# Optimization experiments

Measured on AMD Instinct MI355X. Metric: run time of the kernel, lower is better.

## Reference

```python
import jax, jax.numpy as jnp
import numpy as np

B, S_T, P, D = 2, 8, 1369, 1024
S_STUDENT = 4
R = 128    # num_ref_samples
NS = 128   # num_shared_samples
K = 4      # topk
STUDENT_FRAMES = (0, 2, 4, 6)
EXTRA_FRAMES = (1, 3, 5, 7)   # teacher-only frames
HUBER_DELTA = 1.0
W1 = W2 = W3 = 1.0


def setup_inputs() -> dict:
    key = jax.random.key(0)
    k1, k2, k3, k4 = jax.random.split(key, 4)
    teacher_feats = jax.random.normal(k1, (B, S_T, P, D), dtype=jnp.float32)
    student_feats = jax.random.normal(k2, (B, S_STUDENT, P, D), dtype=jnp.float32)
    ref_perm = jax.random.permutation(k3, P)[:R].astype(jnp.int32)
    shared_perm = jax.random.permutation(k4, P)[:NS].astype(jnp.int32)
    return {"teacher_feats": teacher_feats, "student_feats": student_feats,
            "ref_perm": ref_perm, "shared_perm": shared_perm}


def _unit(x, eps):
    # F.normalize(x, dim=-1, eps=eps)
    n = jnp.linalg.norm(x, axis=-1, keepdims=True)
    return x / jnp.maximum(n, eps)


def _huber(pred, target):
    d = pred - target
    ad = jnp.abs(d)
    return jnp.where(ad < HUBER_DELTA, 0.5 * d * d, HUBER_DELTA * (ad - 0.5 * HUBER_DELTA))


def reference(teacher_feats, student_feats, ref_perm, shared_perm):
    t = jax.lax.stop_gradient(teacher_feats)  # teacher is always detached
    eps = 1e-8

    ref_t = t[:, STUDENT_FRAMES[0], ref_perm, :]        # [B,R,D]
    ref_s = student_feats[:, 0, ref_perm, :]            # [B,R,D]

    # top-K most similar teacher patches across extra frames
    extra_t = t[:, jnp.array(EXTRA_FRAMES)].reshape(B, len(EXTRA_FRAMES) * P, D)  # [B,M,D]
    sim = jnp.einsum('brd,bmd->brm', _unit(ref_t, 1e-12), _unit(extra_t, 1e-12))
    _, idx = jax.lax.top_k(sim, K)                      # [B,R,K]
    sim_high = jnp.take_along_axis(
        extra_t, idx.reshape(B, R * K)[:, :, None], axis=1).reshape(B, R, K, D)

    # vertex-ref / vertex-simhigh legs that don't depend on the shared frame
    b1_t = _unit(sim_high - ref_t[:, :, None, :], eps)  # [B,R,K,D]
    b1_s = _unit(sim_high - ref_s[:, :, None, :], eps)
    u2_t = _unit(ref_t[:, :, None, :] - sim_high, eps)  # [B,R,K,D]
    u2_s = _unit(ref_s[:, :, None, :] - sim_high, eps)

    s1 = jnp.float32(0.0)
    s2 = jnp.float32(0.0)
    s3 = jnp.float32(0.0)
    for f, t_idx in enumerate(STUDENT_FRAMES[1:]):
        sh_t = t[:, t_idx, shared_perm, :]              # [B,S,D]
        sh_s = student_feats[:, f + 1, shared_perm, :]  # [B,S,D]

        # angle1: vertex = ref; cos(shared-ref, simhigh-ref)
        a1_t = jnp.einsum('brsd,brkd->brsk', _unit(sh_t[:, None] - ref_t[:, :, None], eps), b1_t)
        a1_s = jnp.einsum('brsd,brkd->brsk', _unit(sh_s[:, None] - ref_s[:, :, None], eps), b1_s)
        s1 = s1 + _huber(a1_s, jax.lax.stop_gradient(a1_t)).sum()

        # angle2: vertex = sim_high; cos(ref-simhigh, shared-simhigh)
        v2_t = _unit(sh_t[:, None, :, None, :] - sim_high[:, :, None], eps)  # [B,R,S,K,D]
        v2_s = _unit(sh_s[:, None, :, None, :] - sim_high[:, :, None], eps)
        a2_t = jnp.einsum('brkd,brskd->brsk', u2_t, v2_t)
        a2_s = jnp.einsum('brkd,brskd->brsk', u2_s, v2_s)
        s2 = s2 + _huber(a2_s, jax.lax.stop_gradient(a2_t)).sum()

        # angle3: vertex = shared; cos(ref-shared, simhigh-shared)
        u3_t = _unit(ref_t[:, :, None] - sh_t[:, None], eps)                 # [B,R,S,D]
        u3_s = _unit(ref_s[:, :, None] - sh_s[:, None], eps)
        v3_t = _unit(sim_high[:, :, None] - sh_t[:, None, :, None, :], eps)  # [B,R,S,K,D]
        v3_s = _unit(sim_high[:, :, None] - sh_s[:, None, :, None, :], eps)
        a3_t = jnp.einsum('brsd,brskd->brsk', u3_t, v3_t)
        a3_s = jnp.einsum('brsd,brskd->brsk', u3_s, v3_s)
        s3 = s3 + _huber(a3_s, jax.lax.stop_gradient(a3_t)).sum()

    total = B * R * NS * K * len(STUDENT_FRAMES[1:])
    return W1 * s1 / total + W2 * s2 / total + W3 * s3 / total
```

## Files before the change

### kernel.cpp

```cpp
#include <hip/hip_runtime.h>
#include <float.h>

#define B_  2
#define ST_ 8
#define SS_ 4
#define P_  1369
#define D_  1024
#define R_  128
#define NS_ 128
#define K_  4
#define M_  5476

#define OFF_INVN  0u
#define OFF_REFT  11008u
#define OFF_REFS  (OFF_REFT + 262144u)
#define OFF_PRRT  (OFF_REFS + 262144u)
#define OFF_PRRS  (OFF_PRRT + 256u)
#define OFF_IDX   (OFF_PRRS + 256u)
#define OFF_PRST  (OFF_IDX + 1024u)
#define OFF_PRSS  (OFF_PRST + 1024u)
#define OFF_PSS   (OFF_PRSS + 1024u)
#define OFF_IB1T  (OFF_PSS + 1024u)
#define OFF_IB1S  (OFF_IB1T + 1024u)
#define OFF_NSH   (OFF_IB1S + 1024u)
#define OFF_CANDV (OFF_NSH + 1536u)
#define OFF_CANDI (OFF_CANDV + 4096u)
#define OFF_C     (OFF_CANDI + 4096u)
#define CP_       1401856u

#define NA_BLOCKS 2738
#define NB_BLOCKS 384
#define NC_BLOCKS 256

__device__ __forceinline__ float dot4(const float4 a, const float4 b) {
  return a.x*b.x + a.y*b.y + a.z*b.z + a.w*b.w;
}

__global__ __launch_bounds__(256) void k_prep0(const float* __restrict__ teacher,
                                               const float* __restrict__ student,
                                               const int* __restrict__ ref_perm,
                                               const int* __restrict__ shared_perm,
                                               float* __restrict__ invn,
                                               float* __restrict__ nsh,
                                               float* __restrict__ reft,
                                               float* __restrict__ refs,
                                               float* __restrict__ prrt,
                                               float* __restrict__ prrs) {
  const int bid = blockIdx.x;
  const int t = threadIdx.x;
  if (bid < NA_BLOCKS) {
    int row = bid * 4 + (t >> 6);
    int lane = t & 63;
    if (row >= B_ * M_) return;
    int b = row / M_, m = row % M_;
    int j = m / P_, p = m % P_;
    const float* src = teacher + (((size_t)b * ST_ + 1 + 2 * j) * P_ + p) * D_;
    float s = 0.f;
    #pragma unroll
    for (int it = 0; it < 4; ++it) {
      float4 v = *(const float4*)(src + (it * 64 + lane) * 4);
      s += dot4(v, v);
    }
    for (int o = 32; o; o >>= 1) s += __shfl_down(s, o);
    if (lane == 0) invn[row] = 1.f / fmaxf(sqrtf(s), 1e-12f);
  } else if (bid < NA_BLOCKS + NB_BLOCKS) {
    int row = (bid - NA_BLOCKS) * 4 + (t >> 6);
    int lane = t & 63;
    if (row >= 2 * B_ * 3 * NS_) return;
    int rid = row % (B_ * 3 * NS_);
    int is_stu = row / (B_ * 3 * NS_);
    int b = rid / (3 * NS_);
    int rem = rid % (3 * NS_);
    int f = rem / NS_, s = rem % NS_;
    int p = shared_perm[s];
    const float* src = is_stu
        ? student + (((size_t)b * SS_ + 1 + f) * P_ + p) * D_
        : teacher + (((size_t)b * ST_ + 2 + 2 * f) * P_ + p) * D_;
    float acc = 0.f;
    #pragma unroll
    for (int it = 0; it < 4; ++it) {
      float4 v = *(const float4*)(src + (it * 64 + lane) * 4);
      acc += dot4(v, v);
    }
    for (int o = 32; o; o >>= 1) acc += __shfl_down(acc, o);
    if (lane == 0) nsh[row] = acc;
  } else {
    int br = bid - (NA_BLOCKS + NB_BLOCKS);
    int b = br / R_, r = br % R_;
    int p = ref_perm[r];
    const float* st = teacher + (((size_t)b * ST_ + 0) * P_ + p) * D_;
    const float* ss = student + (((size_t)b * SS_ + 0) * P_ + p) * D_;
    float* dt = reft + (size_t)br * D_;
    float* dsp = refs + (size_t)br * D_;
    float4 vt = *(const float4*)(st + t * 4);
    float4 vs = *(const float4*)(ss + t * 4);
    *(float4*)(dt + t * 4) = vt;
    *(float4*)(dsp + t * 4) = vs;
    float at = dot4(vt, vt);
    float as = dot4(vs, vs);
    for (int o = 32; o; o >>= 1) { at += __shfl_down(at, o); as += __shfl_down(as, o); }
    __shared__ float red[16];
    int w = t >> 6, lane = t & 63;
    if (lane == 0) { red[w] = at; red[8 + w] = as; }
    __syncthreads();
    if (t == 0) {
      prrt[br] = red[0] + red[1] + red[2] + red[3];
      prrs[br] = red[8] + red[9] + red[10] + red[11];
    }
  }
}

__global__ __launch_bounds__(256) void k_sim_gemm(const float* __restrict__ teacher,
                                                  const float* __restrict__ reft,
                                                  float* __restrict__ Cp) {
  const int bid = blockIdx.x;
  const int kq  = bid & 3;
  const int rest = bid >> 2;
  const int b   = rest / 172;
  const int rem = rest % 172;
  const int rt  = rem / 86;
  const int mt  = rem % 86;
  const int r0 = rt * 64, m0 = mt * 64;
  __shared__ __align__(16) float Al[32 * 68];
  __shared__ __align__(16) float El[32 * 68];
  const int t = threadIdx.x;
  const int tx = t & 15, ty = t >> 4;
  const int lr = t >> 3;
  const int lk = (t & 7) * 4;
  const float* arow0 = reft + (size_t)(b * R_ + r0 + lr) * D_;
  const float* arow1 = reft + (size_t)(b * R_ + r0 + 32 + lr) * D_;
  const float* erow0; const float* erow1; bool ev0, ev1;
  {
    int m = m0 + lr; ev0 = m < M_;
    int mm = ev0 ? m : 0; int j = mm / P_, p = mm % P_;
    erow0 = teacher + (((size_t)b * ST_ + 1 + 2 * j) * P_ + p) * D_;
    m = m0 + 32 + lr; ev1 = m < M_;
    mm = ev1 ? m : 0; j = mm / P_; p = mm % P_;
    erow1 = teacher + (((size_t)b * ST_ + 1 + 2 * j) * P_ + p) * D_;
  }
  float acc[4][4];
  #pragma unroll
  for (int i = 0; i < 4; ++i)
    #pragma unroll
    for (int j = 0; j < 4; ++j) acc[i][j] = 0.f;

  const int kbeg = kq * 256, kend = kbeg + 256;
  for (int kc = kbeg; kc < kend; kc += 32) {
    __syncthreads();
    float4 a0 = *(const float4*)(arow0 + kc + lk);
    float4 a1 = *(const float4*)(arow1 + kc + lk);
    float4 e0 = ev0 ? *(const float4*)(erow0 + kc + lk) : make_float4(0, 0, 0, 0);
    float4 e1 = ev1 ? *(const float4*)(erow1 + kc + lk) : make_float4(0, 0, 0, 0);
    Al[(lk + 0) * 68 + lr] = a0.x; Al[(lk + 1) * 68 + lr] = a0.y;
    Al[(lk + 2) * 68 + lr] = a0.z; Al[(lk + 3) * 68 + lr] = a0.w;
    Al[(lk + 0) * 68 + 32 + lr] = a1.x; Al[(lk + 1) * 68 + 32 + lr] = a1.y;
    Al[(lk + 2) * 68 + 32 + lr] = a1.z; Al[(lk + 3) * 68 + 32 + lr] = a1.w;
    El[(lk + 0) * 68 + lr] = e0.x; El[(lk + 1) * 68 + lr] = e0.y;
    El[(lk + 2) * 68 + lr] = e0.z; El[(lk + 3) * 68 + lr] = e0.w;
    El[(lk + 0) * 68 + 32 + lr] = e1.x; El[(lk + 1) * 68 + 32 + lr] = e1.y;
    El[(lk + 2) * 68 + 32 + lr] = e1.z; El[(lk + 3) * 68 + 32 + lr] = e1.w;
    __syncthreads();
    #pragma unroll
    for (int kk = 0; kk < 32; ++kk) {
      float4 av = *(const float4*)&Al[kk * 68 + ty * 4];
      float4 ev = *(const float4*)&El[kk * 68 + tx * 4];
      acc[0][0] += av.x * ev.x; acc[0][1] += av.x * ev.y; acc[0][2] += av.x * ev.z; acc[0][3] += av.x * ev.w;
      acc[1][0] += av.y * ev.x; acc[1][1] += av.y * ev.y; acc[1][2] += av.y * ev.z; acc[1][3] += av.y * ev.w;
      acc[2][0] += av.z * ev.x; acc[2][1] += av.z * ev.y; acc[2][2] += av.z * ev.z; acc[2][3] += av.z * ev.w;
      acc[3][0] += av.w * ev.x; acc[3][1] += av.w * ev.y; acc[3][2] += av.w * ev.z; acc[3][3] += av.w * ev.w;
    }
  }
  const int mbase = m0 + tx * 4;
  float* cbase = Cp + (size_t)kq * CP_;
  #pragma unroll
  for (int i = 0; i < 4; ++i) {
    int r = r0 + ty * 4 + i;
    float* crow = cbase + (size_t)(b * R_ + r) * M_;
    if (mbase + 3 < M_) {
      *(float4*)(crow + mbase) = make_float4(acc[i][0], acc[i][1], acc[i][2], acc[i][3]);
    } else {
      if (mbase + 0 < M_) crow[mbase + 0] = acc[i][0];
      if (mbase + 1 < M_) crow[mbase + 1] = acc[i][1];
      if (mbase + 2 < M_) crow[mbase + 2] = acc[i][2];
      if (mbase + 3 < M_) crow[mbase + 3] = acc[i][3];
    }
  }
}

__device__ __forceinline__ void topk_insert(float v, int m, float bv[4], int bi[4]) {
  bool better3 = (v > bv[3]) || (v == bv[3] && m < bi[3]);
  if (!better3) return;
  int pos = 3;
  while (pos > 0) {
    bool better = (v > bv[pos - 1]) || (v == bv[pos - 1] && m < bi[pos - 1]);
    if (better) { bv[pos] = bv[pos - 1]; bi[pos] = bi[pos - 1]; --pos; }
    else break;
  }
  bv[pos] = v; bi[pos] = m;
}

__global__ __launch_bounds__(256) void k_topk1(const float* __restrict__ Cp,
                                               const float* __restrict__ invn,
                                               float* __restrict__ candv,
                                               int* __restrict__ candi) {
  int bid = blockIdx.x;
  int br = bid >> 2, q = bid & 3;
  int b = br / R_;
  const float* r0 = Cp + 0 * (size_t)CP_ + (size_t)br * M_;
  const float* r1 = Cp + 1 * (size_t)CP_ + (size_t)br * M_;
  const float* r2 = Cp + 2 * (size_t)CP_ + (size_t)br * M_;
  const float* r3 = Cp + 3 * (size_t)CP_ + (size_t)br * M_;
  const float* w = invn + (size_t)b * M_;
  const int mbeg = q * 1369, mend = mbeg + 1369;
  int t = threadIdx.x;
  float bv[4] = {-FLT_MAX, -FLT_MAX, -FLT_MAX, -FLT_MAX};
  int   bi[4] = {0x7fffffff, 0x7fffffff, 0x7fffffff, 0x7fffffff};
  for (int m = mbeg + t; m < mend; m += 256) {
    float v = ((r0[m] + r1[m]) + (r2[m] + r3[m])) * w[m];
    topk_insert(v, m, bv, bi);
  }
  #pragma unroll
  for (int o = 1; o < 64; o <<= 1) {
    float ov[4]; int oi[4];
    #pragma unroll
    for (int qq = 0; qq < 4; ++qq) {
      ov[qq] = __shfl_xor(bv[qq], o);
      oi[qq] = __shfl_xor(bi[qq], o);
    }
    #pragma unroll
    for (int qq = 0; qq < 4; ++qq) topk_insert(ov[qq], oi[qq], bv, bi);
  }
  __shared__ float sv[16];
  __shared__ int   si[16];
  int wv = t >> 6, lane = t & 63;
  if (lane == 0) {
    #pragma unroll
    for (int qq = 0; qq < 4; ++qq) { sv[wv * 4 + qq] = bv[qq]; si[wv * 4 + qq] = bi[qq]; }
  }
  __syncthreads();
  if (t == 0) {
    float tv[4] = {-FLT_MAX, -FLT_MAX, -FLT_MAX, -FLT_MAX};
    int   ti[4] = {0x7fffffff, 0x7fffffff, 0x7fffffff, 0x7fffffff};
    #pragma unroll
    for (int e = 0; e < 16; ++e) topk_insert(sv[e], si[e], tv, ti);
    #pragma unroll
    for (int qq = 0; qq < 4; ++qq) { candv[bid * 4 + qq] = tv[qq]; candi[bid * 4 + qq] = ti[qq]; }
  }
}

__global__ __launch_bounds__(256) void k_prep(const float* __restrict__ teacher,
                                              const float* __restrict__ reft,
                                              const float* __restrict__ refs,
                                              const float* __restrict__ candv,
                                              const int* __restrict__ candi,
                                              int* __restrict__ idxout,
                                              float* __restrict__ prst,
                                              float* __restrict__ prss,
                                              float* __restrict__ pss,
                                              float* __restrict__ ib1t,
                                              float* __restrict__ ib1s) {
  int br = blockIdx.x;
  int b = br / R_;
  int t = threadIdx.x;
  __shared__ int sidx[4];
  if (t < 64) {
    float v = -FLT_MAX; int ix = 0x7fffffff;
    if (t < 16) { v = candv[br * 16 + t]; ix = candi[br * 16 + t]; }
    float bv[4] = {v, -FLT_MAX, -FLT_MAX, -FLT_MAX};
    int   bi[4] = {ix, 0x7fffffff, 0x7fffffff, 0x7fffffff};
    #pragma unroll
    for (int o = 1; o <= 8; o <<= 1) {
      float ov[4]; int oi[4];
      #pragma unroll
      for (int q = 0; q < 4; ++q) {
        ov[q] = __shfl_xor(bv[q], o);
        oi[q] = __shfl_xor(bi[q], o);
      }
      #pragma unroll
      for (int q = 0; q < 4; ++q) topk_insert(ov[q], oi[q], bv, bi);
    }
    if (t == 0) {
      #pragma unroll
      for (int q = 0; q < 4; ++q) { sidx[q] = bi[q]; idxout[br * 4 + q] = bi[q]; }
    }
  }
  __syncthreads();
  int w = t >> 6, lane = t & 63;
  int m = sidx[w];
  int j = m / P_, p = m % P_;
  const float* sim = teacher + (((size_t)b * ST_ + 1 + 2 * j) * P_ + p) * D_;
  const float* rt = reft + (size_t)br * D_;
  const float* rs = refs + (size_t)br * D_;
  float s_ss = 0, s_rt = 0, s_rs = 0, s_dt = 0, s_ds = 0;
  #pragma unroll
  for (int it = 0; it < 4; ++it) {
    int d = (it * 64 + lane) * 4;
    float4 svv = *(const float4*)(sim + d);
    float4 tvv = *(const float4*)(rt + d);
    float4 uvv = *(const float4*)(rs + d);
    s_ss += dot4(svv, svv);
    s_rt += dot4(svv, tvv);
    s_rs += dot4(svv, uvv);
    float4 dt = make_float4(svv.x - tvv.x, svv.y - tvv.y, svv.z - tvv.z, svv.w - tvv.w);
    float4 ds = make_float4(svv.x - uvv.x, svv.y - uvv.y, svv.z - uvv.z, svv.w - uvv.w);
    s_dt += dot4(dt, dt);
    s_ds += dot4(ds, ds);
  }
  for (int o = 32; o; o >>= 1) {
    s_ss += __shfl_down(s_ss, o); s_rt += __shfl_down(s_rt, o); s_rs += __shfl_down(s_rs, o);
    s_dt += __shfl_down(s_dt, o); s_ds += __shfl_down(s_ds, o);
  }
  if (lane == 0) {
    int o = br * 4 + w;
    pss[o] = s_ss; prst[o] = s_rt; prss[o] = s_rs;
    ib1t[o] = 1.f / fmaxf(sqrtf(s_dt), 1e-8f);
    ib1s[o] = 1.f / fmaxf(sqrtf(s_ds), 1e-8f);
  }
}

__device__ __forceinline__ float huber1(float d) {
  float ad = fabsf(d);
  return (ad < 1.0f) ? 0.5f * d * d : (ad - 0.5f);
}

__global__ __launch_bounds__(256) void k_loss(const float* __restrict__ teacher,
                                              const float* __restrict__ student,
                                              const int* __restrict__ shared_perm,
                                              const int* __restrict__ idx,
                                              const float* __restrict__ reft,
                                              const float* __restrict__ refs,
                                              const float* __restrict__ prrt,
                                              const float* __restrict__ prrs,
                                              const float* __restrict__ prst,
                                              const float* __restrict__ prss,
                                              const float* __restrict__ pss,
                                              const float* __restrict__ ib1t,
                                              const float* __restrict__ ib1s,
                                              const float* __restrict__ nsh,
                                              float* __restrict__ out) {
  int br = blockIdx.x, f = blockIdx.y;
  int b = br / R_;
  int tf = 2 + 2 * f;
  int sf = 1 + f;
  __shared__ __align__(16) float Lsim[4][1024];
  __shared__ __align__(16) float Lrt[1024];
  __shared__ __align__(16) float Lrs[1024];
  __shared__ int sperm[128];
  __shared__ float Lns[2][128];
  __shared__ float scal[22];
  __shared__ float wred[4];
  int t = threadIdx.x;
  {
    const float* rt = reft + (size_t)br * D_;
    const float* rs = refs + (size_t)br * D_;
    *(float4*)&Lrt[t * 4] = *(const float4*)(rt + t * 4);
    *(float4*)&Lrs[t * 4] = *(const float4*)(rs + t * 4);
    #pragma unroll
    for (int k = 0; k < 4; ++k) {
      int m = idx[br * 4 + k]; int j = m / P_, p = m % P_;
      const float* sim = teacher + (((size_t)b * ST_ + 1 + 2 * j) * P_ + p) * D_;
      *(float4*)&Lsim[k][t * 4] = *(const float4*)(sim + t * 4);
    }
  }
  if (t < 128) {
    sperm[t] = shared_perm[t];
    int o = (b * 3 + f) * NS_ + t;
    Lns[0][t] = nsh[o];
    Lns[1][t] = nsh[B_ * 3 * NS_ + o];
  }
  if (t < 4) {
    int o = br * 4 + t;
    scal[t] = prst[o]; scal[4 + t] = prss[o]; scal[8 + t] = pss[o];
    scal[12 + t] = ib1t[o]; scal[16 + t] = ib1s[o];
  }
  if (t == 4) scal[20] = prrt[br];
  if (t == 5) scal[21] = prrs[br];
  __syncthreads();

  const int g = t >> 2, gl = t & 3;
  const int s0 = g, s1 = g + 64;
  const int p0 = sperm[s0], p1 = sperm[s1];
  const float* sht0 = teacher + (((size_t)b * ST_ + tf) * P_ + p0) * D_;
  const float* sht1 = teacher + (((size_t)b * ST_ + tf) * P_ + p1) * D_;
  const float* shs0 = student + (((size_t)b * SS_ + sf) * P_ + p0) * D_;
  const float* shs1 = student + (((size_t)b * SS_ + sf) * P_ + p1) * D_;

  float qtA0 = 0, qtA1 = 0, qtA2 = 0, qtA3 = 0, qtrA = 0;
  float qsA0 = 0, qsA1 = 0, qsA2 = 0, qsA3 = 0, qsrA = 0;
  float qtB0 = 0, qtB1 = 0, qtB2 = 0, qtB3 = 0, qtrB = 0;
  float qsB0 = 0, qsB1 = 0, qsB2 = 0, qsB3 = 0, qsrB = 0;
  #pragma unroll 2
  for (int i = 0; i < 64; ++i) {
    int off = i * 16 + gl * 4;
    float4 a0 = *(const float4*)(sht0 + off);
    float4 a1 = *(const float4*)(sht1 + off);
    float4 c0 = *(const float4*)(shs0 + off);
    float4 c1 = *(const float4*)(shs1 + off);
    float4 v0 = *(const float4*)&Lsim[0][off];
    float4 v1 = *(const float4*)&Lsim[1][off];
    float4 v2 = *(const float4*)&Lsim[2][off];
    float4 v3 = *(const float4*)&Lsim[3][off];
    float4 r1 = *(const float4*)&Lrt[off];
    float4 r2 = *(const float4*)&Lrs[off];
    qtA0 += dot4(a0, v0); qtA1 += dot4(a0, v1); qtA2 += dot4(a0, v2); qtA3 += dot4(a0, v3);
    qtrA += dot4(a0, r1);
    qsA0 += dot4(c0, v0); qsA1 += dot4(c0, v1); qsA2 += dot4(c0, v2); qsA3 += dot4(c0, v3);
    qsrA += dot4(c0, r2);
    qtB0 += dot4(a1, v0); qtB1 += dot4(a1, v1); qtB2 += dot4(a1, v2); qtB3 += dot4(a1, v3);
    qtrB += dot4(a1, r1);
    qsB0 += dot4(c1, v0); qsB1 += dot4(c1, v1); qsB2 += dot4(c1, v2); qsB3 += dot4(c1, v3);
    qsrB += dot4(c1, r2);
  }
  #pragma unroll
  for (int o = 1; o <= 2; o <<= 1) {
    qtA0 += __shfl_xor(qtA0, o); qtA1 += __shfl_xor(qtA1, o);
    qtA2 += __shfl_xor(qtA2, o); qtA3 += __shfl_xor(qtA3, o);
    qtrA += __shfl_xor(qtrA, o);
    qsA0 += __shfl_xor(qsA0, o); qsA1 += __shfl_xor(qsA1, o);
    qsA2 += __shfl_xor(qsA2, o); qsA3 += __shfl_xor(qsA3, o);
    qsrA += __shfl_xor(qsrA, o);
    qtB0 += __shfl_xor(qtB0, o); qtB1 += __shfl_xor(qtB1, o);
    qtB2 += __shfl_xor(qtB2, o); qtB3 += __shfl_xor(qtB3, o);
    qtrB += __shfl_xor(qtrB, o);
    qsB0 += __shfl_xor(qsB0, o); qsB1 += __shfl_xor(qsB1, o);
    qsB2 += __shfl_xor(qsB2, o); qsB3 += __shfl_xor(qsB3, o);
    qsrB += __shfl_xor(qsrB, o);
  }
  const int k = gl;
  const float Prs_t = scal[k], Prs_s = scal[4 + k], Pss_k = scal[8 + k];
  const float ibt = scal[12 + k], ibs = scal[16 + k];
  const float Prr_t = scal[20], Prr_s = scal[21];

  auto epi = [&](float qsim, float qsimS, float qref, float qrefS,
                 float qss, float qssS) -> float {
    float n1sq = qss - 2.f * qref + Prr_t;
    float i1 = 1.f / fmaxf(sqrtf(fmaxf(n1sq, 0.f)), 1e-8f);
    float n2sq = qss - 2.f * qsim + Pss_k;
    float i2 = 1.f / fmaxf(sqrtf(fmaxf(n2sq, 0.f)), 1e-8f);
    float a1t = (qsim - qref - Prs_t + Prr_t) * ibt * i1;
    float a2t = -(qsim - Pss_k - qref + Prs_t) * ibt * i2;
    float a3t = (qss - qsim - qref + Prs_t) * i1 * i2;
    float n1sqS = qssS - 2.f * qrefS + Prr_s;
    float i1s = 1.f / fmaxf(sqrtf(fmaxf(n1sqS, 0.f)), 1e-8f);
    float n2sqS = qssS - 2.f * qsimS + Pss_k;
    float i2s = 1.f / fmaxf(sqrtf(fmaxf(n2sqS, 0.f)), 1e-8f);
    float a1s = (qsimS - qrefS - Prs_s + Prr_s) * ibs * i1s;
    float a2s = -(qsimS - Pss_k - qrefS + Prs_s) * ibs * i2s;
    float a3s = (qssS - qsimS - qrefS + Prs_s) * i1s * i2s;
    return huber1(a1s - a1t) + huber1(a2s - a2t) + huber1(a3s - a3t);
  };

  float qsimA  = (gl == 0) ? qtA0 : (gl == 1) ? qtA1 : (gl == 2) ? qtA2 : qtA3;
  float qsimSA = (gl == 0) ? qsA0 : (gl == 1) ? qsA1 : (gl == 2) ? qsA2 : qsA3;
  float qsimB  = (gl == 0) ? qtB0 : (gl == 1) ? qtB1 : (gl == 2) ? qtB2 : qtB3;
  float qsimSB = (gl == 0) ? qsB0 : (gl == 1) ? qsB1 : (gl == 2) ? qsB2 : qsB3;

  float lacc = epi(qsimA, qsimSA, qtrA, qsrA, Lns[0][s0], Lns[1][s0])
             + epi(qsimB, qsimSB, qtrB, qsrB, Lns[0][s1], Lns[1][s1]);

  int w = t >> 6, lane = t & 63;
  for (int o = 32; o; o >>= 1) lacc += __shfl_down(lacc, o);
  if (lane == 0) wred[w] = lacc;
  __syncthreads();
  if (t == 0) {
    float ssum = wred[0] + wred[1] + wred[2] + wred[3];
    atomicAdd(out, ssum * (1.0f / 393216.0f));
  }
}

extern "C" void kernel_launch(void* const* d_in, const int* in_sizes, int n_in,
                              void* d_out, int out_size, void* d_ws, size_t ws_size,
                              hipStream_t stream) {
  const float* teacher = (const float*)d_in[0];
  const float* student = (const float*)d_in[1];
  const int* ref_perm = (const int*)d_in[2];
  const int* shared_perm = (const int*)d_in[3];
  float* ws = (float*)d_ws;
  float* invn = ws + OFF_INVN;
  float* reft = ws + OFF_REFT;
  float* refs = ws + OFF_REFS;
  float* prrt = ws + OFF_PRRT;
  float* prrs = ws + OFF_PRRS;
  int*   idx  = (int*)(ws + OFF_IDX);
  float* prst = ws + OFF_PRST;
  float* prss = ws + OFF_PRSS;
  float* pss  = ws + OFF_PSS;
  float* ib1t = ws + OFF_IB1T;
  float* ib1s = ws + OFF_IB1S;
  float* nsh  = ws + OFF_NSH;
  float* candv = ws + OFF_CANDV;
  int*   candi = (int*)(ws + OFF_CANDI);
  float* Cp   = ws + OFF_C;

  hipMemsetAsync(d_out, 0, sizeof(float), stream);

  k_prep0<<<NA_BLOCKS + NB_BLOCKS + NC_BLOCKS, 256, 0, stream>>>(
      teacher, student, ref_perm, shared_perm, invn, nsh, reft, refs, prrt, prrs);
  k_sim_gemm<<<1376, 256, 0, stream>>>(teacher, reft, Cp);
  k_topk1<<<1024, 256, 0, stream>>>(Cp, invn, candv, candi);
  k_prep<<<B_ * R_, 256, 0, stream>>>(teacher, reft, refs, candv, candi, idx,
                                      prst, prss, pss, ib1t, ib1s);
  k_loss<<<dim3(B_ * R_, 3), 256, 0, stream>>>(teacher, student, shared_perm, idx,
                                               reft, refs, prrt, prrs,
                                               prst, prss, pss, ib1t, ib1s,
                                               nsh, (float*)d_out);
}
```

Measured before the change: 305.4 us.

## Fuse extra-frame norm computation into sim GEMM and split K eightfold

```diff
diff --git a/kernel.cpp b/kernel.cpp
--- a/kernel.cpp
+++ b/kernel.cpp
@@ -10,9 +10,9 @@
 #define NS_ 128
 #define K_  4
 #define M_  5476
-
-#define OFF_INVN  0u
-#define OFF_REFT  11008u
+#define BM_ 10952u
+
+#define OFF_REFT  0u
 #define OFF_REFS  (OFF_REFT + 262144u)
 #define OFF_PRRT  (OFF_REFS + 262144u)
 #define OFF_PRRS  (OFF_PRRT + 256u)
@@ -25,10 +25,10 @@
 #define OFF_NSH   (OFF_IB1S + 1024u)
 #define OFF_CANDV (OFF_NSH + 1536u)
 #define OFF_CANDI (OFF_CANDV + 4096u)
-#define OFF_C     (OFF_CANDI + 4096u)
+#define OFF_NSQ   (OFF_CANDI + 4096u)
+#define OFF_C     (OFF_NSQ + 87616u)
 #define CP_       1401856u
 
-#define NA_BLOCKS 2738
 #define NB_BLOCKS 384
 #define NC_BLOCKS 256
 
@@ -40,7 +40,6 @@
                                                const float* __restrict__ student,
                                                const int* __restrict__ ref_perm,
                                                const int* __restrict__ shared_perm,
-                                               float* __restrict__ invn,
                                                float* __restrict__ nsh,
                                                float* __restrict__ reft,
                                                float* __restrict__ refs,
@@ -48,23 +47,8 @@
                                                float* __restrict__ prrs) {
   const int bid = blockIdx.x;
   const int t = threadIdx.x;
-  if (bid < NA_BLOCKS) {
+  if (bid < NB_BLOCKS) {
     int row = bid * 4 + (t >> 6);
-    int lane = t & 63;
-    if (row >= B_ * M_) return;
-    int b = row / M_, m = row % M_;
-    int j = m / P_, p = m % P_;
-    const float* src = teacher + (((size_t)b * ST_ + 1 + 2 * j) * P_ + p) * D_;
-    float s = 0.f;
-    #pragma unroll
-    for (int it = 0; it < 4; ++it) {
-      float4 v = *(const float4*)(src + (it * 64 + lane) * 4);
-      s += dot4(v, v);
-    }
-    for (int o = 32; o; o >>= 1) s += __shfl_down(s, o);
-    if (lane == 0) invn[row] = 1.f / fmaxf(sqrtf(s), 1e-12f);
-  } else if (bid < NA_BLOCKS + NB_BLOCKS) {
-    int row = (bid - NA_BLOCKS) * 4 + (t >> 6);
     int lane = t & 63;
     if (row >= 2 * B_ * 3 * NS_) return;
     int rid = row % (B_ * 3 * NS_);
@@ -85,7 +69,7 @@
     for (int o = 32; o; o >>= 1) acc += __shfl_down(acc, o);
     if (lane == 0) nsh[row] = acc;
   } else {
-    int br = bid - (NA_BLOCKS + NB_BLOCKS);
+    int br = bid - NB_BLOCKS;
     int b = br / R_, r = br % R_;
     int p = ref_perm[r];
     const float* st = teacher + (((size_t)b * ST_ + 0) * P_ + p) * D_;
@@ -112,15 +96,16 @@
 
 __global__ __launch_bounds__(256) void k_sim_gemm(const float* __restrict__ teacher,
                                                   const float* __restrict__ reft,
-                                                  float* __restrict__ Cp) {
+                                                  float* __restrict__ Cp,
+                                                  float* __restrict__ nsq) {
   const int bid = blockIdx.x;
-  const int kq  = bid & 3;
-  const int rest = bid >> 2;
+  const int kq  = bid & 7;
+  const int rest = bid >> 3;
   const int b   = rest / 172;
   const int rem = rest % 172;
-  const int rt  = rem / 86;
+  const int rtb = rem / 86;
   const int mt  = rem % 86;
-  const int r0 = rt * 64, m0 = mt * 64;
+  const int r0 = rtb * 64, m0 = mt * 64;
   __shared__ __align__(16) float Al[32 * 68];
   __shared__ __align__(16) float El[32 * 68];
   const int t = threadIdx.x;
@@ -143,14 +128,24 @@
   for (int i = 0; i < 4; ++i)
     #pragma unroll
     for (int j = 0; j < 4; ++j) acc[i][j] = 0.f;
-
-  const int kbeg = kq * 256, kend = kbeg + 256;
+  float nsq0 = 0.f, nsq1 = 0.f;
+
+  const int kbeg = kq * 128, kend = kbeg + 128;
   for (int kc = kbeg; kc < kend; kc += 32) {
     __syncthreads();
     float4 a0 = *(const float4*)(arow0 + kc + lk);
     float4 a1 = *(const float4*)(arow1 + kc + lk);
     float4 e0 = ev0 ? *(const float4*)(erow0 + kc + lk) : make_float4(0, 0, 0, 0);
     float4 e1 = ev1 ? *(const float4*)(erow1 + kc + lk) : make_float4(0, 0, 0, 0);
+    if (rtb == 0) {
+      float d0 = dot4(e0, e0), d1 = dot4(e1, e1);
+      #pragma unroll
+      for (int o = 1; o <= 4; o <<= 1) {
+        d0 += __shfl_xor(d0, o);
+        d1 += __shfl_xor(d1, o);
+      }
+      nsq0 += d0; nsq1 += d1;
+    }
     Al[(lk + 0) * 68 + lr] = a0.x; Al[(lk + 1) * 68 + lr] = a0.y;
     Al[(lk + 2) * 68 + lr] = a0.z; Al[(lk + 3) * 68 + lr] = a0.w;
     Al[(lk + 0) * 68 + 32 + lr] = a1.x; Al[(lk + 1) * 68 + 32 + lr] = a1.y;
@@ -169,6 +164,13 @@
       acc[2][0] += av.z * ev.x; acc[2][1] += av.z * ev.y; acc[2][2] += av.z * ev.z; acc[2][3] += av.z * ev.w;
       acc[3][0] += av.w * ev.x; acc[3][1] += av.w * ev.y; acc[3][2] += av.w * ev.z; acc[3][3] += av.w * ev.w;
     }
+  }
+  if (rtb == 0 && (t & 7) == 0) {
+    float* nq = nsq + (size_t)kq * BM_ + (size_t)b * M_;
+    int mA = m0 + lr;
+    if (mA < M_) nq[mA] = nsq0;
+    int mB = m0 + 32 + lr;
+    if (mB < M_) nq[mB] = nsq1;
   }
   const int mbase = m0 + tx * 4;
   float* cbase = Cp + (size_t)kq * CP_;
@@ -200,24 +202,27 @@
 }
 
 __global__ __launch_bounds__(256) void k_topk1(const float* __restrict__ Cp,
-                                               const float* __restrict__ invn,
+                                               const float* __restrict__ nsq,
                                                float* __restrict__ candv,
                                                int* __restrict__ candi) {
   int bid = blockIdx.x;
   int br = bid >> 2, q = bid & 3;
   int b = br / R_;
-  const float* r0 = Cp + 0 * (size_t)CP_ + (size_t)br * M_;
-  const float* r1 = Cp + 1 * (size_t)CP_ + (size_t)br * M_;
-  const float* r2 = Cp + 2 * (size_t)CP_ + (size_t)br * M_;
-  const float* r3 = Cp + 3 * (size_t)CP_ + (size_t)br * M_;
-  const float* w = invn + (size_t)b * M_;
+  const float* crow = Cp + (size_t)br * M_;
+  const float* nrow = nsq + (size_t)b * M_;
   const int mbeg = q * 1369, mend = mbeg + 1369;
   int t = threadIdx.x;
   float bv[4] = {-FLT_MAX, -FLT_MAX, -FLT_MAX, -FLT_MAX};
   int   bi[4] = {0x7fffffff, 0x7fffffff, 0x7fffffff, 0x7fffffff};
   for (int m = mbeg + t; m < mend; m += 256) {
-    float v = ((r0[m] + r1[m]) + (r2[m] + r3[m])) * w[m];
-    topk_insert(v, m, bv, bi);
+    float v = 0.f, n = 0.f;
+    #pragma unroll
+    for (int q8 = 0; q8 < 8; ++q8) {
+      v += crow[(size_t)q8 * CP_ + m];
+      n += nrow[(size_t)q8 * BM_ + m];
+    }
+    float inv = 1.f / fmaxf(sqrtf(n), 1e-12f);
+    topk_insert(v * inv, m, bv, bi);
   }
   #pragma unroll
   for (int o = 1; o < 64; o <<= 1) {
@@ -476,7 +481,6 @@
   const int* ref_perm = (const int*)d_in[2];
   const int* shared_perm = (const int*)d_in[3];
   float* ws = (float*)d_ws;
-  float* invn = ws + OFF_INVN;
   float* reft = ws + OFF_REFT;
   float* refs = ws + OFF_REFS;
   float* prrt = ws + OFF_PRRT;
@@ -490,14 +494,15 @@
   float* nsh  = ws + OFF_NSH;
   float* candv = ws + OFF_CANDV;
   int*   candi = (int*)(ws + OFF_CANDI);
+  float* nsq  = ws + OFF_NSQ;
   float* Cp   = ws + OFF_C;
 
   hipMemsetAsync(d_out, 0, sizeof(float), stream);
 
-  k_prep0<<<NA_BLOCKS + NB_BLOCKS + NC_BLOCKS, 256, 0, stream>>>(
-      teacher, student, ref_perm, shared_perm, invn, nsh, reft, refs, prrt, prrs);
-  k_sim_gemm<<<1376, 256, 0, stream>>>(teacher, reft, Cp);
-  k_topk1<<<1024, 256, 0, stream>>>(Cp, invn, candv, candi);
+  k_prep0<<<NB_BLOCKS + NC_BLOCKS, 256, 0, stream>>>(
+      teacher, student, ref_perm, shared_perm, nsh, reft, refs, prrt, prrs);
+  k_sim_gemm<<<2752, 256, 0, stream>>>(teacher, reft, Cp, nsq);
+  k_topk1<<<1024, 256, 0, stream>>>(Cp, nsq, candv, candi);
   k_prep<<<B_ * R_, 256, 0, stream>>>(teacher, reft, refs, candv, candi, idx,
                                       prst, prss, pss, ib1t, ib1s);
   k_loss<<<dim3(B_ * R_, 3), 256, 0, stream>>>(teacher, student, shared_perm, idx,
```

After: 294.4 us. 3.6% less time.
